# Performance work log

Hardware: AMD Instinct MI355X
Metric: run time of the kernel (lower is better)

## Reference

```python
import jax, jax.numpy as jnp
import numpy as np

EPS = 1e-6
N_HEADS, N_KV = 16, 4


def rmsnorm(x, w):
    return x * jax.lax.rsqrt(jnp.mean(x * x, axis=-1, keepdims=True) + EPS) * w


def setup_inputs() -> dict:
    key = jax.random.key(0)
    ks = jax.random.split(key, 9)
    B, T, D, F = 2, 2048, 2048, 8192
    KVD = N_KV * (D // N_HEADS)
    s = lambda k, shape, fan: (jax.random.normal(k, shape, jnp.float32) * (fan ** -0.5))
    return {
        "x": jax.random.normal(ks[0], (B, T, D), jnp.float32),
        "norm1_w": jnp.ones((D,), jnp.float32),
        "norm2_w": jnp.ones((D,), jnp.float32),
        "Wq": s(ks[1], (D, D), D),
        "Wk": s(ks[2], (D, KVD), D),
        "Wv": s(ks[3], (D, KVD), D),
        "Wo": s(ks[4], (D, D), D),
        "Wc": s(ks[5], (D, D), D),
        "W1": s(ks[6], (D, F), D),
        "W2": s(ks[7], (F, D), F),
        "W3": s(ks[8], (D, F), D),
    }


def reference(x, norm1_w, norm2_w, Wq, Wk, Wv, Wo, Wc, W1, W2, W3):
    B, T, D = x.shape
    dh = D // N_HEADS          # 128
    G = N_HEADS // N_KV        # groups per kv head
    scale = dh ** -0.5

    xn = rmsnorm(x, norm1_w)
    q = xn @ Wq                               # [B,T,D]
    pos = q @ Wc                              # CoPE stand-in: contextual positional bias on Q
    q = (q + pos).reshape(B, T, N_KV, G, dh)  # group q heads under their kv head
    k = (xn @ Wk).reshape(B, T, N_KV, dh)
    v = (xn @ Wv).reshape(B, T, N_KV, dh)

    # GQA without repeat_interleave: contract each group against shared K/V
    scores = jnp.einsum('bqkgd,bskd->bkgqs', q, k) * scale   # [B,KV,G,T,T]
    i = jnp.arange(T)
    causal = i[:, None] >= i[None, :]
    scores = jnp.where(causal, scores, -jnp.inf)
    w = jax.nn.softmax(scores, axis=-1)
    att = jnp.einsum('bkgqs,bskd->bqkgd', w, v).reshape(B, T, D)

    x = x + att @ Wo
    xn2 = rmsnorm(x, norm2_w)
    x = x + (jax.nn.silu(xn2 @ W1) * (xn2 @ W3)) @ W2
    return x
```

## Files before the change

### kernel.cpp

```cpp
#include <hip/hip_runtime.h>
#include <hip/hip_bf16.h>

typedef __attribute__((ext_vector_type(8))) short short8;
typedef __attribute__((ext_vector_type(4))) float floatx4;
typedef unsigned short ushort_t;

__device__ inline float b2f(ushort_t s) {
    return __uint_as_float(((unsigned int)s) << 16);
}
__device__ inline ushort_t f2b(float f) {
    unsigned int u = __float_as_uint(f);
    unsigned int r = 0x7fff + ((u >> 16) & 1);
    return (ushort_t)((u + r) >> 16);
}
__device__ inline unsigned int cvtpk(float lo, float hi) {
    unsigned int r;
    asm("v_cvt_pk_bf16_f32 %0, %1, %2" : "=v"(r) : "v"(lo), "v"(hi));
    return r;
}
__device__ inline void load8(const float* p, float* f) {
    float4 a = *(const float4*)p;
    float4 b = *(const float4*)(p + 4);
    f[0] = a.x; f[1] = a.y; f[2] = a.z; f[3] = a.w;
    f[4] = b.x; f[5] = b.y; f[6] = b.z; f[7] = b.w;
}
__device__ inline void gload16(const ushort_t* g, ushort_t* l) {
    __builtin_amdgcn_global_load_lds(
        (const __attribute__((address_space(1))) unsigned int*)g,
        (__attribute__((address_space(3))) unsigned int*)l, 16, 0, 0);
}
__device__ inline void lbar() {
    asm volatile("s_waitcnt lgkmcnt(0)" ::: "memory");
    __builtin_amdgcn_s_barrier();
    asm volatile("" ::: "memory");
}
__device__ inline void drainbar() {
    asm volatile("s_waitcnt vmcnt(0) lgkmcnt(0)" ::: "memory");
    __builtin_amdgcn_s_barrier();
    asm volatile("" ::: "memory");
}

__global__ __launch_bounds__(256) void transpose_all(
    const float* __restrict__ s0, const float* __restrict__ s1,
    const float* __restrict__ s2, const float* __restrict__ s3,
    const float* __restrict__ s4, const float* __restrict__ s5,
    const float* __restrict__ s6, const float* __restrict__ s7,
    ushort_t* d0, ushort_t* d1, ushort_t* d2, ushort_t* d3,
    ushort_t* d4, ushort_t* d5, ushort_t* d6, ushort_t* d7,
    const float* __restrict__ xin, const float* __restrict__ n1w,
    ushort_t* __restrict__ xnout) {
    int id = blockIdx.x;
    int t = threadIdx.x;
    if (id >= 15872) {
        int row = id - 15872;
        const float* xr = xin + (size_t)row * 2048;
        float f[8];
        load8(xr + t * 8, f);
        float ss = 0.f;
#pragma unroll
        for (int i = 0; i < 8; ++i) ss += f[i] * f[i];
#pragma unroll
        for (int m = 1; m < 64; m <<= 1) ss += __shfl_xor(ss, m);
        __shared__ float wsum[4];
        if ((t & 63) == 0) wsum[t >> 6] = ss;
        __syncthreads();
        float tot = wsum[0] + wsum[1] + wsum[2] + wsum[3];
        float r = rsqrtf(tot / 2048.f + 1e-6f);
        float wf[8];
        load8(n1w + t * 8, wf);
        ushort_t o[8];
#pragma unroll
        for (int i = 0; i < 8; ++i) o[i] = f2b(f[i] * r * wf[i]);
        *(uint4*)(xnout + (size_t)row * 2048 + t * 8) = *(const uint4*)o;
        return;
    }
    const float* src; ushort_t* dst; int K, N;
    if (id < 1024)       { src = s0; dst = d0; K = 2048; N = 2048; }
    else if (id < 1280)  { id -= 1024;  src = s1; dst = d1; K = 2048; N = 512; }
    else if (id < 1536)  { id -= 1280;  src = s2; dst = d2; K = 2048; N = 512; }
    else if (id < 2560)  { id -= 1536;  src = s3; dst = d3; K = 2048; N = 2048; }
    else if (id < 3584)  { id -= 2560;  src = s4; dst = d4; K = 2048; N = 2048; }
    else if (id < 7680)  { id -= 3584;  src = s5; dst = d5; K = 2048; N = 8192; }
    else if (id < 11776) { id -= 7680;  src = s6; dst = d6; K = 2048; N = 8192; }
    else                 { id -= 11776; src = s7; dst = d7; K = 8192; N = 2048; }
    int tn = N >> 6;
    int kb = (id / tn) * 64, nb = (id % tn) * 64;
    __shared__ ushort_t tile[64][65];
#pragma unroll
    for (int i = 0; i < 4; ++i) {
        int r = (t >> 4) + i * 16;
        int c = (t & 15) * 4;
        float4 v = *(const float4*)(src + (size_t)(kb + r) * N + nb + c);
        tile[c + 0][r] = f2b(v.x);
        tile[c + 1][r] = f2b(v.y);
        tile[c + 2][r] = f2b(v.z);
        tile[c + 3][r] = f2b(v.w);
    }
    __syncthreads();
#pragma unroll
    for (int i = 0; i < 2; ++i) {
        int s = t + i * 256;
        int n = s >> 3, kc = (s & 7) * 8;
        ushort_t o[8];
#pragma unroll
        for (int j = 0; j < 8; ++j) o[j] = tile[n][kc + j];
        *(uint4*)(dst + (size_t)(nb + n) * K + kb + kc) = *(const uint4*)o;
    }
}

__global__ __launch_bounds__(256) void rmsnorm_kernel(const float* __restrict__ x,
                                                      const float* __restrict__ w,
                                                      ushort_t* __restrict__ out, int D) {
    int row = blockIdx.x;
    int t = threadIdx.x;
    const float* xr = x + (size_t)row * D;
    float f[8];
    load8(xr + t * 8, f);
    float ss = 0.f;
#pragma unroll
    for (int i = 0; i < 8; ++i) ss += f[i] * f[i];
#pragma unroll
    for (int m = 1; m < 64; m <<= 1) ss += __shfl_xor(ss, m);
    __shared__ float wsum[4];
    if ((t & 63) == 0) wsum[t >> 6] = ss;
    __syncthreads();
    float tot = wsum[0] + wsum[1] + wsum[2] + wsum[3];
    float r = rsqrtf(tot / (float)D + 1e-6f);
    float wf[8];
    load8(w + t * 8, wf);
    ushort_t o[8];
#pragma unroll
    for (int i = 0; i < 8; ++i) o[i] = f2b(f[i] * r * wf[i]);
    *(uint4*)(out + (size_t)row * D + t * 8) = *(const uint4*)o;
}

__global__ __launch_bounds__(256) void reduce_out(const ushort_t* __restrict__ p,
                                                  const float* __restrict__ resid,
                                                  float* __restrict__ out, int n) {
    int stride = gridDim.x * 256;
    for (int i = blockIdx.x * 256 + threadIdx.x; i * 8 < n; i += stride) {
        int i8 = i * 8;
        uint4 a = *(const uint4*)(p + i8);
        uint4 b = *(const uint4*)(p + n + i8);
        const ushort_t* ae = (const ushort_t*)&a;
        const ushort_t* be = (const ushort_t*)&b;
        float rr[8];
        load8(resid + i8, rr);
        float o[8];
#pragma unroll
        for (int j = 0; j < 8; ++j) o[j] = b2f(ae[j]) + b2f(be[j]) + rr[j];
        *(float4*)(out + i8) = make_float4(o[0], o[1], o[2], o[3]);
        *(float4*)(out + i8 + 4) = make_float4(o[4], o[5], o[6], o[7]);
    }
}

__global__ __launch_bounds__(256) void attn_merge(const ushort_t* __restrict__ Pb,
                                                  const float* __restrict__ Mb,
                                                  const float* __restrict__ Lb,
                                                  ushort_t* __restrict__ out) {
    const int PSZ = 32 * 2048 * 128;
    int t = threadIdx.x;
    int r = blockIdx.x * 16 + (t >> 4);
    int d0 = (t & 15) * 8;
    float m1 = Mb[r], l1 = Lb[r];
    float m2 = Mb[65536 + r], l2 = Lb[65536 + r];
    float ms = fmaxf(m1, m2);
    float w1 = l1 * __expf(m1 - ms);
    float w2 = l2 * __expf(m2 - ms);
    float inv = 1.f / (w1 + w2);
    w1 *= inv; w2 *= inv;
    uint4 a = *(const uint4*)(Pb + (size_t)r * 128 + d0);
    uint4 b = *(const uint4*)(Pb + (size_t)PSZ + (size_t)r * 128 + d0);
    const ushort_t* ae = (const ushort_t*)&a;
    const ushort_t* be = (const ushort_t*)&b;
    int bh = r >> 11, qrow = r & 2047;
    int bb = bh >> 4, h = bh & 15;
    ushort_t o[8];
#pragma unroll
    for (int j = 0; j < 8; ++j) o[j] = f2b(b2f(ae[j]) * w1 + b2f(be[j]) * w2);
    *(uint4*)(out + ((size_t)(bb * 2048 + qrow) * 2048) + h * 128 + d0) = *(const uint4*)o;
}

__device__ inline void vm6() { asm volatile("s_waitcnt vmcnt(6)" ::: "memory"); }
__device__ inline void vm4() { asm volatile("s_waitcnt vmcnt(4)" ::: "memory"); }

template <int MODE>
__global__ __launch_bounds__(512, 2) void gemm8(const ushort_t* __restrict__ A,
                                                const ushort_t* __restrict__ Bt,
                                                const ushort_t* __restrict__ aux,
                                                const float* __restrict__ aux2,
                                                void* __restrict__ Cv,
                                                void* __restrict__ C2v,
                                                void* __restrict__ C3v,
                                                int M, int N, int Ksub, int lda) {
    __shared__ __align__(16) ushort_t Lds[2 * 32768];
    const int tid = threadIdx.x;
    const int wv = tid >> 6, lane = tid & 63;
    const int l16 = lane & 15, l4 = lane >> 4;
    const int wr = wv >> 2, wc = wv & 3;
    int nwg = gridDim.x;
    int per = nwg >> 3;
    int wg = (blockIdx.x & 7) * per + (blockIdx.x >> 3);
    int mtiles = M >> 8;
    int bx = wg & (mtiles - 1);
    int by = wg / mtiles;
    int bm = bx << 8, bn = by << 8;
    int koff = blockIdx.y * Ksub;

    const int sr = tid >> 3;
    const int scol = (((tid & 7) ^ (sr & 7)) << 3);
    const ushort_t* gA = A + (size_t)(bm + sr) * lda + scol + koff;
    const ushort_t* gB = Bt + (size_t)(bn + sr) * lda + scol + koff;
    ushort_t* ldsw = Lds + wv * 512;

    const int ktiles = Ksub >> 6;
    const int niter = ktiles >> 1;
    const int km = ktiles - 1;

#define STG_A(slot, j, kt) gload16(gA + (size_t)((j) * 64) * lda + ((kt) << 6), ldsw + (slot) * 32768 + (j) * 4096)
#define STG_B(slot, j, kt) gload16(gB + (size_t)((j) * 64) * lda + ((kt) << 6), ldsw + (slot) * 32768 + 16384 + (j) * 4096)

    STG_A(0, 0, 0); STG_A(0, 2, 0); STG_A(0, 1, 0); STG_A(0, 3, 0);
    STG_B(0, 0, 0); STG_B(0, 1, 0); STG_B(0, 2, 0); STG_B(0, 3, 0);
    STG_A(1, 0, 1); STG_A(1, 2, 1);
    STG_B(1, 0, 1); STG_B(1, 1, 1); STG_B(1, 2, 1); STG_B(1, 3, 1);
    vm6();
    asm volatile("" ::: "memory");
    __builtin_amdgcn_s_barrier();

    const int lx = l4 ^ (l16 & 7);
    floatx4 acc[8][4] = {};
    short8 aR[4][2], bR[4][2];

#define DSA(slot, mh) { _Pragma("unroll") for (int m = 0; m < 4; ++m) { \
    _Pragma("unroll") for (int kk = 0; kk < 2; ++kk) \
      aR[m][kk] = *(const short8*)(Lds + (slot) * 32768 + \
          (wr * 128 + (mh) * 64 + m * 16 + l16) * 64 + ((lx ^ (kk << 2)) << 3)); } }
#define DSB(slot, nh) { _Pragma("unroll") for (int n = 0; n < 2; ++n) { \
    _Pragma("unroll") for (int kk = 0; kk < 2; ++kk) \
      bR[(nh) * 2 + n][kk] = *(const short8*)(Lds + (slot) * 32768 + 16384 + \
          (wc * 64 + ((nh) * 2 + n) * 16 + l16) * 64 + ((lx ^ (kk << 2)) << 3)); } }
#define QUAD(mh, nlo) { _Pragma("unroll") for (int m = 0; m < 4; ++m) \
    _Pragma("unroll") for (int n = 0; n < 2; ++n) \
    _Pragma("unroll") for (int kk = 0; kk < 2; ++kk) \
      acc[(mh) * 4 + m][(nlo) + n] = __builtin_amdgcn_mfma_f32_16x16x32_bf16( \
          aR[m][kk], bR[(nlo) + n][kk], acc[(mh) * 4 + m][(nlo) + n], 0, 0, 0); }
#define PHASE(DS, ST, MH, NLO, VM) { \
    DS; ST; \
    asm volatile("" ::: "memory"); \
    __builtin_amdgcn_s_barrier(); \
    asm volatile("s_waitcnt lgkmcnt(0)" ::: "memory"); \
    __builtin_amdgcn_sched_barrier(0); \
    __builtin_amdgcn_s_setprio(1); \
    QUAD(MH, NLO); \
    __builtin_amdgcn_s_setprio(0); \
    VM; \
    asm volatile("" ::: "memory"); \
    __builtin_amdgcn_s_barrier(); }

    for (int it = 0; it < niter; ++it) {
        int t1 = 2 * it + 1;
        int t2 = (2 * it + 2) & km;
        int t3 = (2 * it + 3) & km;
        PHASE({ DSA(0, 0); DSB(0, 0); }, { STG_A(1, 1, t1); STG_A(1, 3, t1); }, 0, 0, );
        PHASE({ DSB(0, 1); },            { STG_A(0, 0, t2); STG_A(0, 2, t2); }, 0, 2, );
        PHASE({ DSA(0, 1); },            { STG_B(0, 0, t2); STG_B(0, 1, t2); }, 1, 2, );
        PHASE({ },                       { STG_B(0, 2, t2); STG_B(0, 3, t2); }, 1, 0, vm6(); );
        PHASE({ DSA(1, 0); DSB(1, 0); }, { STG_A(0, 1, t2); STG_A(0, 3, t2); }, 0, 0, );
        PHASE({ DSB(1, 1); },            { STG_A(1, 0, t3); STG_A(1, 2, t3); }, 0, 2, );
        PHASE({ DSA(1, 1); },            { STG_B(1, 0, t3); STG_B(1, 1, t3); }, 1, 2, );
        PHASE({ },                       { STG_B(1, 2, t3); STG_B(1, 3, t3); }, 1, 0, vm6(); );
    }

    drainbar();
    ushort_t* Cs = Lds;

    if (MODE == 6 && bn >= 2560) {
#pragma unroll
        for (int mi = 0; mi < 8; ++mi)
#pragma unroll
            for (int ni = 0; ni < 4; ++ni)
#pragma unroll
                for (int r = 0; r < 4; ++r) {
                    int row = wr * 128 + mi * 16 + l4 * 4 + r;
                    int col = wc * 64 + ni * 16 + l16;
                    int pch = (row >> 3) ^ (col & 7);
                    Cs[col * 256 + pch * 8 + (row & 7)] = f2b(acc[mi][ni][r]);
                }
        lbar();
        {
            int ch = tid & 31;
            int c0 = tid >> 5;
            ushort_t* Vb = (ushort_t*)C3v;
#pragma unroll
            for (int cg = 0; cg < 16; ++cg) {
                int col = cg * 16 + c0;
                int pch = ch ^ (col & 7);
                uint4 cv4 = *(const uint4*)(Cs + col * 256 + pch * 8);
                *(uint4*)(Vb + (size_t)(bn - 2560 + col) * 4096 + bm + ch * 8) = cv4;
            }
        }
    } else {
#pragma unroll
        for (int mi = 0; mi < 8; ++mi)
#pragma unroll
            for (int ni = 0; ni < 4; ++ni)
#pragma unroll
                for (int r = 0; r < 4; ++r) {
                    int row = wr * 128 + mi * 16 + l4 * 4 + r;
                    int col = wc * 64 + ni * 16 + l16;
                    int pch = (col >> 3) ^ (row & 7);
                    Cs[row * 256 + pch * 8 + (col & 7)] = f2b(acc[mi][ni][r]);
                }
        lbar();
        {
            int ch = tid & 31;
            int r0 = tid >> 5;
            ushort_t* dst;
            int ostride, ocoff;
            if (MODE == 6) {
                if (bn < 2048) { dst = (ushort_t*)Cv;  ostride = 2048; ocoff = bn; }
                else           { dst = (ushort_t*)C2v; ostride = 512;  ocoff = bn - 2048; }
            } else {
                dst = (ushort_t*)Cv; ostride = N; ocoff = bn;
            }
#pragma unroll
            for (int rg = 0; rg < 16; ++rg) {
                int row = rg * 16 + r0;
                int pch = ch ^ (row & 7);
                uint4 cv4 = *(const uint4*)(Cs + row * 256 + pch * 8);
                size_t g = (size_t)(bm + row) * ostride + ocoff + ch * 8;
                if (MODE == 3) g += (size_t)blockIdx.y * M * N;
                if (MODE == 2) {
                    uint4 av4 = *(const uint4*)(aux + g);
                    const ushort_t* ce = (const ushort_t*)&cv4;
                    const ushort_t* ae = (const ushort_t*)&av4;
                    ushort_t o[8];
#pragma unroll
                    for (int j = 0; j < 8; ++j) {
                        float hh = b2f(ae[j]);
                        o[j] = f2b((hh / (1.f + __expf(-hh))) * b2f(ce[j]));
                    }
                    *(uint4*)(dst + g) = *(const uint4*)o;
                } else {
                    *(uint4*)(dst + g) = cv4;
                }
            }
        }
    }
#undef STG_A
#undef STG_B
#undef DSA
#undef DSB
#undef QUAD
#undef PHASE
}

template <int MODE>
__global__ __launch_bounds__(512, 1) void gemm8h(const ushort_t* __restrict__ A,
                                                 const ushort_t* __restrict__ Bt,
                                                 const ushort_t* __restrict__ aux,
                                                 const float* __restrict__ aux2,
                                                 void* __restrict__ Cv,
                                                 int M, int N, int K) {
    __shared__ __align__(16) ushort_t Lds[2 * 24576];
    const int tid = threadIdx.x;
    const int wv = tid >> 6, lane = tid & 63;
    const int l16 = lane & 15, l4 = lane >> 4;
    const int wr = wv >> 2, wc = wv & 3;
    int nwg = gridDim.x;
    int per = nwg >> 3;
    int wg = (blockIdx.x & 7) * per + (blockIdx.x >> 3);
    int mtiles = M >> 7;
    int bx = wg & (mtiles - 1);
    int by = wg / mtiles;
    int bm = bx << 7, bn = by << 8;

    const int sr = tid >> 3;
    const int scol = (((tid & 7) ^ (sr & 7)) << 3);
    const ushort_t* gA = A + (size_t)(bm + sr) * K + scol;
    const ushort_t* gB = Bt + (size_t)(bn + sr) * K + scol;
    ushort_t* ldsw = Lds + wv * 512;

    const int ktiles = K >> 6;
    const int niter = ktiles >> 1;
    const int km = ktiles - 1;

#define HSTG_A(slot, j, kt) gload16(gA + (size_t)((j) * 64) * K + ((kt) << 6), ldsw + (slot) * 24576 + (j) * 4096)
#define HSTG_B(slot, j, kt) gload16(gB + (size_t)((j) * 64) * K + ((kt) << 6), ldsw + (slot) * 24576 + 8192 + (j) * 4096)

    HSTG_A(0, 0, 0); HSTG_A(0, 1, 0);
    HSTG_B(0, 0, 0); HSTG_B(0, 1, 0); HSTG_B(0, 2, 0); HSTG_B(0, 3, 0);
    HSTG_A(1, 0, 1); HSTG_A(1, 1, 1);
    HSTG_B(1, 0, 1); HSTG_B(1, 1, 1);
    vm4();
    asm volatile("" ::: "memory");
    __builtin_amdgcn_s_barrier();

    const int lx = l4 ^ (l16 & 7);
    floatx4 acc[4][4] = {};
    short8 aR[2][2], bR[4][2];

#define HDSA(slot, mh) { _Pragma("unroll") for (int m = 0; m < 2; ++m) { \
    _Pragma("unroll") for (int kk = 0; kk < 2; ++kk) \
      aR[m][kk] = *(const short8*)(Lds + (slot) * 24576 + \
          (wr * 64 + (mh) * 32 + m * 16 + l16) * 64 + ((lx ^ (kk << 2)) << 3)); } }
#define HDSB(slot, nh) { _Pragma("unroll") for (int n = 0; n < 2; ++n) { \
    _Pragma("unroll") for (int kk = 0; kk < 2; ++kk) \
      bR[(nh) * 2 + n][kk] = *(const short8*)(Lds + (slot) * 24576 + 8192 + \
          (wc * 64 + ((nh) * 2 + n) * 16 + l16) * 64 + ((lx ^ (kk << 2)) << 3)); } }
#define HQUAD(mh, nlo) { _Pragma("unroll") for (int m = 0; m < 2; ++m) \
    _Pragma("unroll") for (int n = 0; n < 2; ++n) \
    _Pragma("unroll") for (int kk = 0; kk < 2; ++kk) \
      acc[(mh) * 2 + m][(nlo) + n] = __builtin_amdgcn_mfma_f32_16x16x32_bf16( \
          aR[m][kk], bR[(nlo) + n][kk], acc[(mh) * 2 + m][(nlo) + n], 0, 0, 0); }
#define HPHASE(DS, ST, MH, NLO, VM) { \
    DS; ST; \
    asm volatile("" ::: "memory"); \
    __builtin_amdgcn_s_barrier(); \
    asm volatile("s_waitcnt lgkmcnt(0)" ::: "memory"); \
    __builtin_amdgcn_sched_barrier(0); \
    __builtin_amdgcn_s_setprio(1); \
    HQUAD(MH, NLO); \
    __builtin_amdgcn_s_setprio(0); \
    VM; \
    asm volatile("" ::: "memory"); \
    __builtin_amdgcn_s_barrier(); }

    for (int it = 0; it < niter; ++it) {
        int t1 = 2 * it + 1;
        int t2 = (2 * it + 2) & km;
        int t3 = (2 * it + 3) & km;
        HPHASE({ HDSA(0, 0); HDSB(0, 0); }, { HSTG_B(1, 2, t1); HSTG_B(1, 3, t1); }, 0, 0, );
        HPHASE({ HDSB(0, 1); },             { },                                     0, 2, );
        HPHASE({ HDSA(0, 1); },             { HSTG_B(0, 0, t2); HSTG_B(0, 1, t2); }, 1, 2, );
        HPHASE({ },                         { HSTG_B(0, 2, t2); HSTG_B(0, 3, t2); }, 1, 0, vm4(); );
        HPHASE({ HDSA(1, 0); HDSB(1, 0); }, { HSTG_A(0, 0, t2); HSTG_A(0, 1, t2); }, 0, 0, );
        HPHASE({ HDSB(1, 1); },             { },                                     0, 2, );
        HPHASE({ HDSA(1, 1); },             { HSTG_B(1, 0, t3); HSTG_B(1, 1, t3); }, 1, 2, );
        HPHASE({ },                         { HSTG_A(1, 0, t3); HSTG_A(1, 1, t3); }, 1, 0, vm4(); );
    }

    if (MODE == 1) {
        drainbar();
        ushort_t* Cs = Lds;
#pragma unroll
        for (int mi = 0; mi < 4; ++mi)
#pragma unroll
            for (int ni = 0; ni < 4; ++ni)
#pragma unroll
                for (int r = 0; r < 4; ++r) {
                    int row = wr * 64 + mi * 16 + l4 * 4 + r;
                    int col = wc * 64 + ni * 16 + l16;
                    int pch = (col >> 3) ^ (row & 7);
                    Cs[row * 256 + pch * 8 + (col & 7)] = f2b(acc[mi][ni][r]);
                }
        lbar();
        {
            int ch = tid & 31;
            int r0 = tid >> 5;
            ushort_t* Cb = (ushort_t*)Cv;
#pragma unroll
            for (int rg = 0; rg < 8; ++rg) {
                int row = rg * 16 + r0;
                int pch = ch ^ (row & 7);
                uint4 cv4 = *(const uint4*)(Cs + row * 256 + pch * 8);
                size_t g = (size_t)(bm + row) * N + bn + ch * 8;
                uint4 av4 = *(const uint4*)(aux + g);
                const ushort_t* ce = (const ushort_t*)&cv4;
                const ushort_t* ae = (const ushort_t*)&av4;
                ushort_t o[8];
#pragma unroll
                for (int j = 0; j < 8; ++j) o[j] = f2b(b2f(ce[j]) + b2f(ae[j]));
                *(uint4*)(Cb + g) = *(const uint4*)o;
            }
        }
    } else {
#pragma unroll
        for (int mi = 0; mi < 4; ++mi)
#pragma unroll
            for (int ni = 0; ni < 4; ++ni)
#pragma unroll
                for (int r = 0; r < 4; ++r) {
                    int row = bm + wr * 64 + mi * 16 + l4 * 4 + r;
                    int col = bn + wc * 64 + ni * 16 + l16;
                    size_t idx = (size_t)row * N + col;
                    ((float*)Cv)[idx] = acc[mi][ni][r] + aux2[idx];
                }
    }
#undef HSTG_A
#undef HSTG_B
#undef HDSA
#undef HDSB
#undef HQUAD
#undef HPHASE
}

#define QB 256
#define SB 64

__global__ __launch_bounds__(512, 1) void attn_kernel(const ushort_t* __restrict__ Q,
                                                      const ushort_t* __restrict__ Kb,
                                                      const ushort_t* __restrict__ VbT,
                                                      ushort_t* __restrict__ Pb,
                                                      float* __restrict__ Mb,
                                                      float* __restrict__ Lb, int Tlen) {
    const int D = 2048, KVD = 512, dh = 128;
    const int MTOK = 4096;
    const int PSZ = 32 * 2048 * 128;
    int p = blockIdx.x, h = blockIdx.y, b = blockIdx.z;
    int jsp = (p >= 4) ? 1 : 0;
    int kv = h >> 2;
    int t = threadIdx.x, wave = t >> 6, lane = t & 63;
    int l16 = lane & 15, l4 = lane >> 4;
    __shared__ __align__(16) ushort_t LdsAll[45056];
    const float scale = 0.08838834764831845f;
    const ushort_t* Kg = Kb + ((size_t)(b * Tlen) + (t >> 4)) * KVD + kv * dh + (t & 15) * 8;
    const ushort_t* Vg = VbT + (size_t)(kv * dh + (t >> 3)) * MTOK + b * Tlen + (t & 7) * 8;
    const int kw_off = (t >> 4) * 136 + (t & 15) * 8;
    const int vw_off = 17408 + (t >> 3) * 72 + (t & 7) * 8;
    unsigned int* PsB = (unsigned int*)(LdsAll + 26624);

    for (int side = 0; side < 2; ++side) {
        int qt = side ? p : (7 - p);
        if (qt >= 8) qt -= 8;
        int qbase = qt * QB;
        int qw = qbase + wave * 32;
        short8 qf[2][4];
#pragma unroll
        for (int f = 0; f < 2; ++f) {
            const ushort_t* Qrow = Q + ((size_t)(b * Tlen) + qw + f * 16 + l16) * D + h * dh;
#pragma unroll
            for (int kk = 0; kk < 4; ++kk) qf[f][kk] = *(const short8*)(Qrow + kk * 32 + l4 * 8);
        }
        floatx4 o_acc[2][8] = {};
        float m_s[2], l_s[2];
#pragma unroll
        for (int f = 0; f < 2; ++f) { m_s[f] = -1e30f; l_s[f] = 0.f; }
        int half = 2 * qt + 2;
        int st0 = jsp * half;
        int stEnd = st0 + half;
        uint4 kreg[2], vreg[2];
#pragma unroll
        for (int p4 = 0; p4 < 2; ++p4) {
            kreg[p4] = *(const uint4*)(Kg + (size_t)((size_t)st0 * SB + p4 * 32) * KVD);
            vreg[p4] = *(const uint4*)(Vg + (size_t)(p4 * 64) * MTOK + (size_t)st0 * SB);
        }
        lbar();
#pragma unroll
        for (int p4 = 0; p4 < 2; ++p4)
            *(uint4*)(LdsAll + (st0 & 1) * 8704 + kw_off + p4 * 32 * 136) = kreg[p4];
        {
            size_t off = (size_t)(st0 + 1) * SB;
#pragma unroll
            for (int p4 = 0; p4 < 2; ++p4)
                kreg[p4] = *(const uint4*)(Kg + (off + p4 * 32) * KVD);
        }
        for (int st = st0; st < stEnd; ++st) {
            int cur = st & 1;
            int s0 = st * SB;
            lbar();
#pragma unroll
            for (int p4 = 0; p4 < 2; ++p4)
                *(uint4*)(LdsAll + vw_off + p4 * 64 * 72) = vreg[p4];
            if (st + 1 < stEnd) {
#pragma unroll
                for (int p4 = 0; p4 < 2; ++p4)
                    *(uint4*)(LdsAll + (cur ^ 1) * 8704 + kw_off + p4 * 32 * 136) = kreg[p4];
            }
            if (st + 1 < stEnd) {
                size_t off = (size_t)(st + 1) * SB;
#pragma unroll
                for (int p4 = 0; p4 < 2; ++p4)
                    vreg[p4] = *(const uint4*)(Vg + (size_t)(p4 * 64) * MTOK + off);
            }
            if (st + 2 < stEnd) {
                size_t off = (size_t)(st + 2) * SB;
#pragma unroll
                for (int p4 = 0; p4 < 2; ++p4)
                    kreg[p4] = *(const uint4*)(Kg + (off + p4 * 32) * KVD);
            }
            floatx4 sa[2][4] = {};
            __builtin_amdgcn_s_setprio(1);
#pragma unroll
            for (int ss = 0; ss < 4; ++ss)
#pragma unroll
                for (int kk = 0; kk < 4; ++kk) {
                    short8 kf = *(const short8*)(LdsAll + cur * 8704 + (ss * 16 + l16) * 136 + kk * 32 + l4 * 8);
                    sa[0][ss] = __builtin_amdgcn_mfma_f32_16x16x32_bf16(kf, qf[0][kk], sa[0][ss], 0, 0, 0);
                    sa[1][ss] = __builtin_amdgcn_mfma_f32_16x16x32_bf16(kf, qf[1][kk], sa[1][ss], 0, 0, 0);
                }
            __builtin_amdgcn_s_setprio(0);
            short8 pa[2][2];
#pragma unroll
            for (int f = 0; f < 2; ++f) {
                int qcol = qw + f * 16 + l16;
                float sv[4][4];
                float pmax = -INFINITY;
#pragma unroll
                for (int ss = 0; ss < 4; ++ss)
#pragma unroll
                    for (int r = 0; r < 4; ++r) {
                        int krow = s0 + ss * 16 + l4 * 4 + r;
                        float v = sa[f][ss][r] * scale;
                        if (krow > qcol) v = -INFINITY;
                        sv[ss][r] = v;
                        pmax = fmaxf(pmax, v);
                    }
                pmax = fmaxf(pmax, __shfl_xor(pmax, 16));
                pmax = fmaxf(pmax, __shfl_xor(pmax, 32));
                bool skip = __all(pmax <= m_s[f] + 8.f);
                float mn = skip ? m_s[f] : fmaxf(m_s[f], pmax);
                float rsum = 0.f;
#pragma unroll
                for (int ss = 0; ss < 4; ++ss)
#pragma unroll
                    for (int r = 0; r < 4; ++r) {
                        float pv = __expf(sv[ss][r] - mn);
                        sv[ss][r] = pv;
                        rsum += pv;
                    }
                rsum += __shfl_xor(rsum, 16);
                rsum += __shfl_xor(rsum, 32);
                if (skip) {
                    l_s[f] += rsum;
                } else {
                    float esc = __expf(m_s[f] - mn);
                    l_s[f] = l_s[f] * esc + rsum;
                    m_s[f] = mn;
                    float ef[4];
#pragma unroll
                    for (int r = 0; r < 4; ++r) ef[r] = __shfl(esc, l4 * 4 + r);
#pragma unroll
                    for (int c = 0; c < 8; ++c)
#pragma unroll
                        for (int r = 0; r < 4; ++r) o_acc[f][c][r] *= ef[r];
                }
                unsigned int* Pw = PsB + (wave * 2 + f) * 16 * 36;
#pragma unroll
                for (int ss = 0; ss < 4; ++ss) {
                    uint2 pk;
                    pk.x = cvtpk(sv[ss][0], sv[ss][1]);
                    pk.y = cvtpk(sv[ss][2], sv[ss][3]);
                    *(uint2*)&Pw[l16 * 36 + ss * 8 + l4 * 2] = pk;
                }
#pragma unroll
                for (int kk = 0; kk < 2; ++kk) {
                    uint4 pv4 = *(const uint4*)&Pw[l16 * 36 + kk * 16 + l4 * 4];
                    pa[f][kk] = *(const short8*)&pv4;
                }
            }
            lbar();
            __builtin_amdgcn_s_setprio(1);
#pragma unroll
            for (int c = 0; c < 8; ++c)
#pragma unroll
                for (int kk = 0; kk < 2; ++kk) {
                    short8 vf = *(const short8*)(LdsAll + 17408 + (c * 16 + l16) * 72 + kk * 32 + l4 * 8);
                    o_acc[0][c] = __builtin_amdgcn_mfma_f32_16x16x32_bf16(pa[0][kk], vf, o_acc[0][c], 0, 0, 0);
                    o_acc[1][c] = __builtin_amdgcn_mfma_f32_16x16x32_bf16(pa[1][kk], vf, o_acc[1][c], 0, 0, 0);
                }
            __builtin_amdgcn_s_setprio(0);
        }
        lbar();
#pragma unroll
        for (int f = 0; f < 2; ++f) {
            if (l4 == 0) {
                int ridx = jsp * 65536 + ((b * 16 + h) << 11) + qw + f * 16 + l16;
                Mb[ridx] = m_s[f];
                Lb[ridx] = l_s[f];
            }
        }
        ushort_t* Osh = LdsAll;
#pragma unroll
        for (int f = 0; f < 2; ++f) {
            float linv[4];
#pragma unroll
            for (int r = 0; r < 4; ++r) {
                float lv = __shfl(l_s[f], l4 * 4 + r);
                linv[r] = (lv > 0.f) ? (1.f / lv) : 0.f;
            }
#pragma unroll
            for (int c = 0; c < 8; ++c)
#pragma unroll
                for (int r = 0; r < 4; ++r)
                    Osh[(wave * 32 + f * 16 + l4 * 4 + r) * 136 + c * 16 + l16] =
                        f2b(o_acc[f][c][r] * linv[r]);
        }
        lbar();
        {
            int orow = t >> 1, occ = (t & 1) * 64;
            const ushort_t* srcp = Osh + orow * 136 + occ;
            ushort_t* dstp = Pb + (size_t)jsp * PSZ +
                             ((size_t)((b * 16 + h)) * 2048 + qbase + orow) * 128 + occ;
#pragma unroll
            for (int k = 0; k < 8; ++k)
                *(uint4*)(dstp + k * 8) = *(const uint4*)(srcp + k * 8);
        }
    }
}

extern "C" void kernel_launch(void* const* d_in, const int* in_sizes, int n_in,
                              void* d_out, int out_size, void* d_ws, size_t ws_size,
                              hipStream_t stream) {
    const float* x   = (const float*)d_in[0];
    const float* n1w = (const float*)d_in[1];
    const float* n2w = (const float*)d_in[2];
    const float* Wq  = (const float*)d_in[3];
    const float* Wk  = (const float*)d_in[4];
    const float* Wv  = (const float*)d_in[5];
    const float* Wo  = (const float*)d_in[6];
    const float* Wc  = (const float*)d_in[7];
    const float* W1  = (const float*)d_in[8];
    const float* W2  = (const float*)d_in[9];
    const float* W3  = (const float*)d_in[10];
    float* out = (float*)d_out;

    const int B = 2, T = 2048, D = 2048, F = 8192, KVD = 512;
    const int M = B * T;
    const size_t XD   = (size_t)M * D * 2;
    const size_t XDF  = (size_t)M * D * 4;
    const size_t KVSZ = (size_t)M * KVD * 2;
    const size_t MF   = (size_t)M * F * 2;
    const size_t WDD  = (size_t)D * D * 2;
    const size_t WQKV = (size_t)(D + 2 * KVD) * D * 2;
    const size_t WDF  = (size_t)D * F * 2;

    char* w = (char*)d_ws;
    ushort_t* xn    = (ushort_t*)(w);
    ushort_t* qtmp  = (ushort_t*)(w + XD);
    ushort_t* qfin  = (ushort_t*)(w + 2 * XD);
    float*    x2f   = (float*)   (w + 3 * XD);
    ushort_t* kbuf  = (ushort_t*)(w + 3 * XD + XDF);
    ushort_t* vbufT = (ushort_t*)(w + 3 * XD + XDF + KVSZ);
    ushort_t* h1    = (ushort_t*)(w + 3 * XD + XDF + 2 * KVSZ);
    char* wt = w + 3 * XD + XDF + 2 * KVSZ + MF;
    ushort_t* WqkvT = (ushort_t*)(wt);
    ushort_t* WcT   = (ushort_t*)(wt + WQKV);
    ushort_t* WoT   = (ushort_t*)(wt + WQKV + WDD);
    ushort_t* W1T   = (ushort_t*)(wt + WQKV + 2 * WDD);
    ushort_t* W3T   = (ushort_t*)(wt + WQKV + 2 * WDD + WDF);
    ushort_t* W2T   = (ushort_t*)(wt + WQKV + 2 * WDD + 2 * WDF);
    ushort_t* Pb = h1;
    float*    Mb = (float*)((char*)h1 + 2 * (size_t)32 * 2048 * 128 * 2);
    float*    Lb = Mb + 2 * 65536;

    dim3 blk(256);
    dim3 blk8(512);

    transpose_all<<<19968, blk, 0, stream>>>(
        Wq, Wk, Wv, Wc, Wo, W1, W3, W2,
        WqkvT, WqkvT + (size_t)2048 * D, WqkvT + (size_t)2560 * D,
        WcT, WoT, W1T, W3T, W2T,
        x, n1w, xn);

    gemm8<6><<<dim3((M / 256) * (3072 / 256)), blk8, 0, stream>>>(
        xn, WqkvT, nullptr, nullptr, qtmp, kbuf, vbufT, M, 3072, D, D);
    gemm8h<1><<<dim3((M / 128) * (D / 256)), blk8, 0, stream>>>(
        qtmp, WcT, qtmp, nullptr, qfin, M, D, D);
    attn_kernel<<<dim3(8, 16, B), blk8, 0, stream>>>(qfin, kbuf, vbufT, Pb, Mb, Lb, T);
    attn_merge<<<4096, blk, 0, stream>>>(Pb, Mb, Lb, qtmp);
    gemm8h<5><<<dim3((M / 128) * (D / 256)), blk8, 0, stream>>>(
        qtmp, WoT, nullptr, x, x2f, M, D, D);
    rmsnorm_kernel<<<M, blk, 0, stream>>>(x2f, n2w, xn, D);
    gemm8<0><<<dim3((M / 256) * (F / 256)), blk8, 0, stream>>>(
        xn, W1T, nullptr, nullptr, h1, nullptr, nullptr, M, F, D, D);
    gemm8<2><<<dim3((M / 256) * (F / 256)), blk8, 0, stream>>>(
        xn, W3T, h1, nullptr, h1, nullptr, nullptr, M, F, D, D);
    gemm8<3><<<dim3((M / 256) * (D / 256), 2), blk8, 0, stream>>>(
        h1, W2T, nullptr, nullptr, xn, nullptr, nullptr, M, D, F / 2, F);
    reduce_out<<<1024, blk, 0, stream>>>(xn, x2f, out, M * D);
}
```

Measured before the change: 725.7 us.

## Fuse W1 and W3 GEMMs into one interleaved GEMM with SwiGLU epilogue

Interleaves the transposed W1 and W3 weights in 128-column blocks so that each 256-wide output tile holds matching gate and up columns. A single GEMM of width 16384 then applies silu(gate)*up in its epilogue and writes h1 directly. This removes one kernel launch, the bf16 write and re-read of the intermediate h1, and the second read of the xn activations. In exchange the epilogue does more math per tile and stores half-width outputs.

```diff
diff --git a/kernel.cpp b/kernel.cpp
--- a/kernel.cpp
+++ b/kernel.cpp
@@ -75,16 +75,19 @@
         return;
     }
     const float* src; ushort_t* dst; int K, N;
+    int rbm = 0;
     if (id < 1024)       { src = s0; dst = d0; K = 2048; N = 2048; }
     else if (id < 1280)  { id -= 1024;  src = s1; dst = d1; K = 2048; N = 512; }
     else if (id < 1536)  { id -= 1280;  src = s2; dst = d2; K = 2048; N = 512; }
     else if (id < 2560)  { id -= 1536;  src = s3; dst = d3; K = 2048; N = 2048; }
     else if (id < 3584)  { id -= 2560;  src = s4; dst = d4; K = 2048; N = 2048; }
-    else if (id < 7680)  { id -= 3584;  src = s5; dst = d5; K = 2048; N = 8192; }
-    else if (id < 11776) { id -= 7680;  src = s6; dst = d6; K = 2048; N = 8192; }
+    else if (id < 7680)  { id -= 3584;  src = s5; dst = d5; K = 2048; N = 8192; rbm = 1; }
+    else if (id < 11776) { id -= 7680;  src = s6; dst = d6; K = 2048; N = 8192; rbm = 2; }
     else                 { id -= 11776; src = s7; dst = d7; K = 8192; N = 2048; }
     int tn = N >> 6;
     int kb = (id / tn) * 64, nb = (id % tn) * 64;
+    int rowbase = nb;
+    if (rbm) rowbase = ((nb >> 7) << 8) + (nb & 127) + ((rbm == 2) ? 128 : 0);
     __shared__ ushort_t tile[64][65];
 #pragma unroll
     for (int i = 0; i < 4; ++i) {
@@ -104,7 +107,7 @@
         ushort_t o[8];
 #pragma unroll
         for (int j = 0; j < 8; ++j) o[j] = tile[n][kc + j];
-        *(uint4*)(dst + (size_t)(nb + n) * K + kb + kc) = *(const uint4*)o;
+        *(uint4*)(dst + (size_t)(rowbase + n) * K + kb + kc) = *(const uint4*)o;
     }
 }
 
@@ -300,6 +303,41 @@
                 *(uint4*)(Vb + (size_t)(bn - 2560 + col) * 4096 + bm + ch * 8) = cv4;
             }
         }
+    } else if (MODE == 7) {
+#pragma unroll
+        for (int mi = 0; mi < 8; ++mi)
+#pragma unroll
+            for (int ni = 0; ni < 4; ++ni)
+#pragma unroll
+                for (int r = 0; r < 4; ++r) {
+                    int row = wr * 128 + mi * 16 + l4 * 4 + r;
+                    int col = wc * 64 + ni * 16 + l16;
+                    int pch = (col >> 3) ^ (row & 7);
+                    Cs[row * 256 + pch * 8 + (col & 7)] = f2b(acc[mi][ni][r]);
+                }
+        lbar();
+        {
+            int ch = tid & 15;
+            int r0 = tid >> 4;
+            ushort_t* Hb = (ushort_t*)Cv;
+#pragma unroll
+            for (int rg = 0; rg < 8; ++rg) {
+                int row = rg * 32 + r0;
+                int pl = ch ^ (row & 7);
+                int pr = (ch + 16) ^ (row & 7);
+                uint4 lv = *(const uint4*)(Cs + row * 256 + pl * 8);
+                uint4 rv = *(const uint4*)(Cs + row * 256 + pr * 8);
+                const ushort_t* le = (const ushort_t*)&lv;
+                const ushort_t* re = (const ushort_t*)&rv;
+                ushort_t o[8];
+#pragma unroll
+                for (int j = 0; j < 8; ++j) {
+                    float a = b2f(le[j]);
+                    o[j] = f2b((a / (1.f + __expf(-a))) * b2f(re[j]));
+                }
+                *(uint4*)(Hb + (size_t)(bm + row) * 8192 + (bn >> 1) + ch * 8) = *(const uint4*)o;
+            }
+        }
     } else {
 #pragma unroll
         for (int mi = 0; mi < 8; ++mi)
@@ -331,20 +369,7 @@
                 uint4 cv4 = *(const uint4*)(Cs + row * 256 + pch * 8);
                 size_t g = (size_t)(bm + row) * ostride + ocoff + ch * 8;
                 if (MODE == 3) g += (size_t)blockIdx.y * M * N;
-                if (MODE == 2) {
-                    uint4 av4 = *(const uint4*)(aux + g);
-                    const ushort_t* ce = (const ushort_t*)&cv4;
-                    const ushort_t* ae = (const ushort_t*)&av4;
-                    ushort_t o[8];
-#pragma unroll
-                    for (int j = 0; j < 8; ++j) {
-                        float hh = b2f(ae[j]);
-                        o[j] = f2b((hh / (1.f + __expf(-hh))) * b2f(ce[j]));
-                    }
-                    *(uint4*)(dst + g) = *(const uint4*)o;
-                } else {
-                    *(uint4*)(dst + g) = cv4;
-                }
+                *(uint4*)(dst + g) = cv4;
             }
         }
     }
@@ -738,8 +763,7 @@
     ushort_t* WqkvT = (ushort_t*)(wt);
     ushort_t* WcT   = (ushort_t*)(wt + WQKV);
     ushort_t* WoT   = (ushort_t*)(wt + WQKV + WDD);
-    ushort_t* W1T   = (ushort_t*)(wt + WQKV + 2 * WDD);
-    ushort_t* W3T   = (ushort_t*)(wt + WQKV + 2 * WDD + WDF);
+    ushort_t* WfT   = (ushort_t*)(wt + WQKV + 2 * WDD);
     ushort_t* W2T   = (ushort_t*)(wt + WQKV + 2 * WDD + 2 * WDF);
     ushort_t* Pb = h1;
     float*    Mb = (float*)((char*)h1 + 2 * (size_t)32 * 2048 * 128 * 2);
@@ -751,7 +775,7 @@
     transpose_all<<<19968, blk, 0, stream>>>(
         Wq, Wk, Wv, Wc, Wo, W1, W3, W2,
         WqkvT, WqkvT + (size_t)2048 * D, WqkvT + (size_t)2560 * D,
-        WcT, WoT, W1T, W3T, W2T,
+        WcT, WoT, WfT, WfT, W2T,
         x, n1w, xn);
 
     gemm8<6><<<dim3((M / 256) * (3072 / 256)), blk8, 0, stream>>>(
@@ -763,10 +787,8 @@
     gemm8h<5><<<dim3((M / 128) * (D / 256)), blk8, 0, stream>>>(
         qtmp, WoT, nullptr, x, x2f, M, D, D);
     rmsnorm_kernel<<<M, blk, 0, stream>>>(x2f, n2w, xn, D);
-    gemm8<0><<<dim3((M / 256) * (F / 256)), blk8, 0, stream>>>(
-        xn, W1T, nullptr, nullptr, h1, nullptr, nullptr, M, F, D, D);
-    gemm8<2><<<dim3((M / 256) * (F / 256)), blk8, 0, stream>>>(
-        xn, W3T, h1, nullptr, h1, nullptr, nullptr, M, F, D, D);
+    gemm8<7><<<dim3((M / 256) * (16384 / 256)), blk8, 0, stream>>>(
+        xn, WfT, nullptr, nullptr, h1, nullptr, nullptr, M, 16384, D, D);
     gemm8<3><<<dim3((M / 256) * (D / 256), 2), blk8, 0, stream>>>(
         h1, W2T, nullptr, nullptr, xn, nullptr, nullptr, M, D, F / 2, F);
     reduce_out<<<1024, blk, 0, stream>>>(xn, x2f, out, M * D);
```

New measurement: 708.9 us. 2.3% less time.
